# Performance work log

Hardware: AMD Instinct MI355X
Metric: run time of the kernel (lower is better)

Reference implementation:

```python
import jax, jax.numpy as jnp
import numpy as np

# ---- constants derived from init_kwargs ----
DETECT_THRESHOLD = 3.0
DETECT_SIGN = -1          # negative spikes
MARGIN_LEFT = 20          # snippet_T1
MARGIN_RIGHT = 20         # snippet_T2
CHANNEL_RADIUS = 100.0
SAMPLING_FREQUENCY = 30000.0
TIME_RADIUS = int(np.ceil(0.5 / 1000.0 * SAMPLING_FREQUENCY))  # = 15
MAX_DETECTIONS = 100000   # static cap for jit-compatible compaction


def setup_inputs() -> dict:
    key = jax.random.key(0)
    k1, k2 = jax.random.split(key)
    traces = jax.random.normal(k1, (150000, 384), dtype=jnp.float32)
    # spread channels over a 2000x2000 um area so radius=100 gives sparse adjacency
    channel_locations = jax.random.uniform(k2, (384, 2), dtype=jnp.float32) * 2000.0
    return {"traces": traces, "channel_locations": channel_locations}


def _detect_mask(traces, channel_locations):
    N, M = traces.shape
    # orientation (detect_sign < 0 -> traces_inv = -traces)
    if DETECT_SIGN > 0:
        traces_inv = traces
    elif DETECT_SIGN == 0:
        traces_inv = jnp.abs(traces)
    else:
        traces_inv = -traces

    # temporal max-pool, kernel 2*TR+1, stride 1, same padding (pads with -inf)
    pool = 2 * TIME_RADIUS + 1
    neg_inf = jnp.float32(-jnp.inf)
    temporal_max = jax.lax.reduce_window(
        traces_inv, neg_inf, jax.lax.max,
        window_dimensions=(pool, 1), window_strides=(1, 1),
        padding=((TIME_RADIUS, TIME_RADIUS), (0, 0)))  # [N, M]

    # channel adjacency from pairwise distances
    diff = channel_locations[:, None, :] - channel_locations[None, :, :]
    dists = jnp.sqrt(jnp.sum(diff * diff, axis=-1))  # [M, M]
    adj = dists <= CHANNEL_RADIUS

    # per-channel masked neighbor max over temporal_max columns -> [N, M]
    # sequential lax.map over channels avoids an N x M x M intermediate
    spatial_max = jax.lax.map(
        lambda row: jnp.max(jnp.where(row[None, :], temporal_max, neg_inf), axis=1),
        adj).T  # [N, M]

    t = jnp.arange(N)
    margin_ok = (t >= MARGIN_LEFT) & (t < N - MARGIN_RIGHT)  # [N]

    valid = ((traces_inv == temporal_max)
             & (traces_inv >= DETECT_THRESHOLD)
             & margin_ok[:, None]
             & (traces_inv >= spatial_max))
    return valid, traces_inv


def reference(traces, channel_locations):
    valid, _ = _detect_mask(traces, channel_locations)
    # row-major nonzero order == stable sort by time (row index)
    times, chans = jnp.nonzero(valid, size=MAX_DETECTIONS, fill_value=-1)
    return times.astype(jnp.int64), chans.astype(jnp.int32)
```

## Files before the change

### kernel.cpp

```cpp
#include <hip/hip_runtime.h>
#include <stdint.h>

#define M_CH       384
#define TR         15
#define MARGIN     20
#define CHUNK_ROWS 16
#define BM_WORDS   192
#define WPR        12

__device__ __forceinline__ uint32_t spread4(uint32_t x) {
    x = (x | (x << 12)) & 0x000F000Fu;
    x = (x | (x << 6))  & 0x03030303u;
    x = (x | (x << 3))  & 0x11111111u;
    return x;
}

__global__ void nbr_kernel(const float* __restrict__ locs,
                           uint32_t* __restrict__ nEntries,
                           uint8_t* __restrict__ entryWord,
                           uint32_t* __restrict__ entryMask) {
    __shared__ float lx[M_CH], ly[M_CH];
    int t = threadIdx.x;
    lx[t] = locs[2 * t];
    ly[t] = locs[2 * t + 1];
    __syncthreads();
    float x = lx[t], y = ly[t];
    uint32_t m[WPR];
    #pragma unroll
    for (int k = 0; k < WPR; ++k) m[k] = 0;
    for (int c = 0; c < M_CH; ++c) {
        float dx = x - lx[c], dy = y - ly[c];
        if (sqrtf(dx * dx + dy * dy) <= 100.0f) m[c >> 5] |= 1u << (c & 31);
    }
    int ne = 0;
    #pragma unroll
    for (int k = 0; k < WPR; ++k) {
        if (m[k]) {
            entryWord[t * WPR + ne] = (uint8_t)k;
            entryMask[t * WPR + ne] = m[k];
            ne++;
        }
    }
    nEntries[t] = (uint32_t)ne;
}

__global__ __launch_bounds__(256)
void cand_kernel(const float* __restrict__ traces, long n4, long nwords,
                 uint32_t* __restrict__ candWords) {
    const int lane = threadIdx.x & 63;
    const long wv = (((long)blockIdx.x * 256) + threadIdx.x) >> 6;
    const long fb = wv * 256;
    uint64_t B00,B01,B02,B03, B10,B11,B12,B13,
             B20,B21,B22,B23, B30,B31,B32,B33;
    {
        float4 v0 = make_float4(0,0,0,0), v1 = v0, v2 = v0, v3 = v0;
        long i0 = fb + 0 * 64 + lane;
        long i1 = fb + 1 * 64 + lane;
        long i2 = fb + 2 * 64 + lane;
        long i3 = fb + 3 * 64 + lane;
        if (i0 < n4) v0 = ((const float4*)traces)[i0];
        if (i1 < n4) v1 = ((const float4*)traces)[i1];
        if (i2 < n4) v2 = ((const float4*)traces)[i2];
        if (i3 < n4) v3 = ((const float4*)traces)[i3];
        B00 = __ballot(v0.x <= -3.0f); B01 = __ballot(v0.y <= -3.0f);
        B02 = __ballot(v0.z <= -3.0f); B03 = __ballot(v0.w <= -3.0f);
        B10 = __ballot(v1.x <= -3.0f); B11 = __ballot(v1.y <= -3.0f);
        B12 = __ballot(v1.z <= -3.0f); B13 = __ballot(v1.w <= -3.0f);
        B20 = __ballot(v2.x <= -3.0f); B21 = __ballot(v2.y <= -3.0f);
        B22 = __ballot(v2.z <= -3.0f); B23 = __ballot(v2.w <= -3.0f);
        B30 = __ballot(v3.x <= -3.0f); B31 = __ballot(v3.y <= -3.0f);
        B32 = __ballot(v3.z <= -3.0f); B33 = __ballot(v3.w <= -3.0f);
    }
    if (lane < 32) {
        int k  = lane >> 3;
        int sh = (lane & 7) * 8;
        uint64_t b0 = (k & 2) ? ((k & 1) ? B30 : B20) : ((k & 1) ? B10 : B00);
        uint64_t b1 = (k & 2) ? ((k & 1) ? B31 : B21) : ((k & 1) ? B11 : B01);
        uint64_t b2 = (k & 2) ? ((k & 1) ? B32 : B22) : ((k & 1) ? B12 : B02);
        uint64_t b3 = (k & 2) ? ((k & 1) ? B33 : B23) : ((k & 1) ? B13 : B03);
        uint32_t w = spread4((uint32_t)(b0 >> sh) & 0xFFu)
                   | (spread4((uint32_t)(b1 >> sh) & 0xFFu) << 1)
                   | (spread4((uint32_t)(b2 >> sh) & 0xFFu) << 2)
                   | (spread4((uint32_t)(b3 >> sh) & 0xFFu) << 3);
        long wIdx = wv * 32 + lane;
        if (wIdx < nwords) candWords[wIdx] = w;
    }
}

__global__ __launch_bounds__(192)
void validate_count_kernel(const float* __restrict__ traces, int N, long nwords,
                           const uint32_t* __restrict__ nEntries,
                           const uint8_t* __restrict__ entryWord,
                           const uint32_t* __restrict__ entryMask,
                           const uint32_t* __restrict__ candWords,
                           uint32_t* __restrict__ validOut,
                           uint32_t* __restrict__ chunkCounts) {
    __shared__ uint32_t red[3];
    const int t = threadIdx.x;
    const long w = (long)blockIdx.x * BM_WORDS + t;
    uint32_t out = 0;
    if (w < nwords) {
        uint32_t word = candWords[w];
        if (word) {
            int r  = (int)(w / WPR);
            int cw = (int)(w - (long)r * WPR);
            if (r >= MARGIN && r < N - MARGIN) {
                out = word;
                uint32_t tmp = word;
                while (tmp) {
                    int bit = __ffs(tmp) - 1;
                    tmp &= tmp - 1;
                    int c = cw * 32 + bit;
                    float raw = traces[(long)r * M_CH + c];
                    int ne = (int)nEntries[c];
                    bool bad = false;
                    for (int k = 0; k < ne; ++k) {
                        int wi = (int)entryWord[c * WPR + k];
                        uint32_t em = entryMask[c * WPR + k];
                        const uint32_t* colp = candWords + (long)(r - TR) * WPR + wi;
                        uint32_t hitRows = 0;
                        #pragma unroll
                        for (int dt = 0; dt < 31; ++dt) {
                            uint32_t h = colp[(long)dt * WPR] & em;
                            hitRows |= (h ? 1u : 0u) << dt;
                        }
                        if (hitRows) {
                            while (hitRows) {
                                int dt = __ffs(hitRows) - 1;
                                hitRows &= hitRows - 1;
                                uint32_t h = colp[(long)dt * WPR] & em;
                                while (h) {
                                    int b2 = __ffs(h) - 1;
                                    h &= h - 1;
                                    float v = traces[(long)(r - TR + dt) * M_CH + wi * 32 + b2];
                                    if (v < raw) bad = true;
                                }
                            }
                            if (bad) break;
                        }
                    }
                    if (bad) out &= ~(1u << bit);
                }
            }
        }
        validOut[w] = out;
    }
    int pc = __popc(out);
    #pragma unroll
    for (int off = 32; off; off >>= 1) pc += __shfl_xor(pc, off, 64);
    if ((t & 63) == 0) red[t >> 6] = (uint32_t)pc;
    __syncthreads();
    if (t == 0) chunkCounts[blockIdx.x] = red[0] + red[1] + red[2];
}

__global__ void scan_kernel(const uint32_t* __restrict__ counts, int n,
                            uint32_t* __restrict__ prefix) {
    __shared__ uint32_t s[256];
    int t = threadIdx.x;
    int per = (n + 255) / 256;
    int lo = t * per, hi = min(lo + per, n);
    uint32_t sum = 0;
    for (int i = lo; i < hi; ++i) sum += counts[i];
    s[t] = sum;
    __syncthreads();
    for (int off = 1; off < 256; off <<= 1) {
        uint32_t v = (t >= off) ? s[t - off] : 0;
        __syncthreads();
        s[t] += v;
        __syncthreads();
    }
    uint32_t run = s[t] - sum;
    for (int i = lo; i < hi; ++i) { prefix[i] = run; run += counts[i]; }
    if (t == 255) prefix[n] = run;
}

__global__ void emit_fill_kernel(const uint32_t* __restrict__ validOut,
                                 const uint32_t* __restrict__ chunkPrefix,
                                 int nchunk, int emitBlocks, int maxdet,
                                 int* __restrict__ times, int* __restrict__ chans) {
    if ((int)blockIdx.x >= emitBlocks) {
        int i = ((int)blockIdx.x - emitBlocks) * 256 + threadIdx.x;
        int total = (int)chunkPrefix[nchunk];
        if (i < maxdet && i >= total) { times[i] = -1; chans[i] = -1; }
        return;
    }
    int wv = threadIdx.x >> 6;
    int lane = threadIdx.x & 63;
    int chunkId = blockIdx.x * 4 + wv;
    if (chunkId >= nchunk) return;

    const uint32_t* wp = validOut + (long)chunkId * BM_WORDS + lane * 3;
    uint32_t b0 = wp[0], b1 = wp[1], b2 = wp[2];
    int local = __popc(b0) + __popc(b1) + __popc(b2);

    int s = local;
    #pragma unroll
    for (int off = 1; off < 64; off <<= 1) {
        int v = __shfl_up(s, off, 64);
        if (lane >= off) s += v;
    }
    int base = (int)chunkPrefix[chunkId] + (s - local);
    int r0 = chunkId * CHUNK_ROWS;

    uint32_t words[3] = { b0, b1, b2 };
    #pragma unroll
    for (int q = 0; q < 3; ++q) {
        uint32_t x = words[q];
        int fbase = (lane * 3 + q) * 32;
        while (x) {
            int b = __ffs(x) - 1;
            x &= x - 1;
            int f = fbase + b;
            int n = f / M_CH;
            int ch = f - n * M_CH;
            if (base < maxdet) {
                times[base] = r0 + n;
                chans[base] = ch;
            }
            base++;
        }
    }
}

extern "C" void kernel_launch(void* const* d_in, const int* in_sizes, int n_in,
                              void* d_out, int out_size, void* d_ws, size_t ws_size,
                              hipStream_t stream) {
    const float* traces = (const float*)d_in[0];
    const float* locs   = (const float*)d_in[1];
    const int M = M_CH;
    const int N = in_sizes[0] / M;
    const long nsamp = (long)N * M;
    const int maxdet = out_size / 2;
    int* times = (int*)d_out;
    int* chans = times + maxdet;

    const long n4     = nsamp / 4;
    const long nwords = nsamp / 32;
    const int  nchunk = (N + CHUNK_ROWS - 1) / CHUNK_ROWS;

    char* ws = (char*)d_ws;
    uint32_t* nEntries    = (uint32_t*)(ws + 0);
    uint8_t*  entryWord   = (uint8_t*)(ws + 1536);
    uint32_t* entryMask   = (uint32_t*)(ws + 6144);
    uint32_t* chunkCounts = (uint32_t*)(ws + 24576);
    uint32_t* chunkPrefix = (uint32_t*)(ws + 62080);
    uint32_t* candWords   = (uint32_t*)(ws + 99584);
    uint32_t* validOut    = (uint32_t*)(ws + 7299584);

    nbr_kernel<<<1, M_CH, 0, stream>>>(locs, nEntries, entryWord, entryMask);

    const long nwaves = (nwords + 31) / 32;
    const int  cblocks = (int)((nwaves + 3) / 4);
    cand_kernel<<<cblocks, 256, 0, stream>>>(traces, n4, nwords, candWords);

    validate_count_kernel<<<nchunk, BM_WORDS, 0, stream>>>(
        traces, N, nwords, nEntries, entryWord, entryMask, candWords,
        validOut, chunkCounts);

    scan_kernel<<<1, 256, 0, stream>>>(chunkCounts, nchunk, chunkPrefix);

    const int emitBlocks = (nchunk + 3) / 4;
    const int fillBlocks = (maxdet + 255) / 256;
    emit_fill_kernel<<<emitBlocks + fillBlocks, 256, 0, stream>>>(
        validOut, chunkPrefix, nchunk, emitBlocks, maxdet, times, chans);
}
```

Baseline: 425.7 us.

## Stage candidate window in LDS, skip self-only checks, fuse neighbor build into cand kernel

The neighbor-mask computation is folded into an extra block of the candidate kernel, which removes one kernel launch. The validate kernel now stages a 46-row window of candidate bitmap words in shared memory and reads neighbourhood bits from there instead of from global memory. It also first ORs all neighbor bits, excluding the sample itself, so that it loads trace values only when a competing candidate exists. This saves launch overhead and global bitmap traffic, at the cost of slightly more shared memory per block and a two-pass loop over neighbor entries.

```diff
diff --git a/kernel.cpp b/kernel.cpp
--- a/kernel.cpp
+++ b/kernel.cpp
@@ -7,6 +7,7 @@
 #define CHUNK_ROWS 16
 #define BM_WORDS   192
 #define WPR        12
+#define WIN_ROWS   46
 
 __device__ __forceinline__ uint32_t spread4(uint32_t x) {
     x = (x | (x << 12)) & 0x000F000Fu;
@@ -15,38 +16,44 @@
     return x;
 }
 
-__global__ void nbr_kernel(const float* __restrict__ locs,
-                           uint32_t* __restrict__ nEntries,
-                           uint8_t* __restrict__ entryWord,
-                           uint32_t* __restrict__ entryMask) {
-    __shared__ float lx[M_CH], ly[M_CH];
-    int t = threadIdx.x;
-    lx[t] = locs[2 * t];
-    ly[t] = locs[2 * t + 1];
-    __syncthreads();
-    float x = lx[t], y = ly[t];
-    uint32_t m[WPR];
-    #pragma unroll
-    for (int k = 0; k < WPR; ++k) m[k] = 0;
-    for (int c = 0; c < M_CH; ++c) {
-        float dx = x - lx[c], dy = y - ly[c];
-        if (sqrtf(dx * dx + dy * dy) <= 100.0f) m[c >> 5] |= 1u << (c & 31);
-    }
-    int ne = 0;
-    #pragma unroll
-    for (int k = 0; k < WPR; ++k) {
-        if (m[k]) {
-            entryWord[t * WPR + ne] = (uint8_t)k;
-            entryMask[t * WPR + ne] = m[k];
-            ne++;
-        }
-    }
-    nEntries[t] = (uint32_t)ne;
-}
-
 __global__ __launch_bounds__(256)
-void cand_kernel(const float* __restrict__ traces, long n4, long nwords,
-                 uint32_t* __restrict__ candWords) {
+void cand_kernel(const float* __restrict__ traces,
+                 const float* __restrict__ locs,
+                 long n4, long nwords, int nbrBlock,
+                 uint32_t* __restrict__ candWords,
+                 uint32_t* __restrict__ nEntries,
+                 uint8_t* __restrict__ entryWord,
+                 uint32_t* __restrict__ entryMask) {
+    if ((int)blockIdx.x >= nbrBlock) {
+        __shared__ float lx[M_CH], ly[M_CH];
+        const int t = threadIdx.x;
+        for (int c = t; c < M_CH; c += 256) {
+            lx[c] = locs[2 * c];
+            ly[c] = locs[2 * c + 1];
+        }
+        __syncthreads();
+        for (int c0 = t; c0 < M_CH; c0 += 256) {
+            float x = lx[c0], y = ly[c0];
+            int ne = 0;
+            for (int k = 0; k < WPR; ++k) {
+                uint32_t mk = 0;
+                #pragma unroll
+                for (int b = 0; b < 32; ++b) {
+                    int c = k * 32 + b;
+                    float dx = x - lx[c], dy = y - ly[c];
+                    if (sqrtf(dx * dx + dy * dy) <= 100.0f) mk |= 1u << b;
+                }
+                if (mk) {
+                    entryWord[c0 * WPR + ne] = (uint8_t)k;
+                    entryMask[c0 * WPR + ne] = mk;
+                    ne++;
+                }
+            }
+            nEntries[c0] = (uint32_t)ne;
+        }
+        return;
+    }
+
     const int lane = threadIdx.x & 63;
     const long wv = (((long)blockIdx.x * 256) + threadIdx.x) >> 6;
     const long fb = wv * 256;
@@ -95,51 +102,77 @@
                            const uint32_t* __restrict__ candWords,
                            uint32_t* __restrict__ validOut,
                            uint32_t* __restrict__ chunkCounts) {
+    __shared__ uint32_t win[WIN_ROWS * WPR];
     __shared__ uint32_t red[3];
     const int t = threadIdx.x;
+    const int r0 = (int)blockIdx.x * CHUNK_ROWS;
+
+    {
+        const long base = (long)(r0 - TR) * WPR;
+        #pragma unroll
+        for (int i0 = 0; i0 < WIN_ROWS * WPR; i0 += 192) {
+            int i = i0 + t;
+            if (i < WIN_ROWS * WPR) {
+                long g = base + i;
+                win[i] = (g >= 0 && g < nwords) ? candWords[g] : 0u;
+            }
+        }
+    }
+    __syncthreads();
+
+    const int lr = t / WPR;
+    const int wi = t - lr * WPR;
+    const int r  = r0 + lr;
     const long w = (long)blockIdx.x * BM_WORDS + t;
+
     uint32_t out = 0;
     if (w < nwords) {
-        uint32_t word = candWords[w];
-        if (word) {
-            int r  = (int)(w / WPR);
-            int cw = (int)(w - (long)r * WPR);
-            if (r >= MARGIN && r < N - MARGIN) {
-                out = word;
-                uint32_t tmp = word;
-                while (tmp) {
-                    int bit = __ffs(tmp) - 1;
-                    tmp &= tmp - 1;
-                    int c = cw * 32 + bit;
+        uint32_t word = win[(lr + TR) * WPR + wi];
+        if (word && r >= MARGIN && r < N - MARGIN) {
+            out = word;
+            uint32_t tmp = word;
+            while (tmp) {
+                int bit = __ffs(tmp) - 1;
+                tmp &= tmp - 1;
+                const int c = wi * 32 + bit;
+                const uint32_t selfbit = 1u << bit;
+                const int ne = (int)nEntries[c];
+
+                uint32_t anyComp = 0;
+                for (int k = 0; k < ne; ++k) {
+                    int wiE = (int)entryWord[c * WPR + k];
+                    uint32_t em = entryMask[c * WPR + k];
+                    const uint32_t* colp = &win[lr * WPR + wiE];
+                    uint32_t orw = 0;
+                    #pragma unroll
+                    for (int dt = 0; dt < 31; ++dt) {
+                        uint32_t h = colp[dt * WPR];
+                        if (dt == TR) h &= (wiE == wi) ? ~selfbit : 0xFFFFFFFFu;
+                        orw |= h & em;
+                    }
+                    anyComp |= orw;
+                }
+
+                if (anyComp) {
                     float raw = traces[(long)r * M_CH + c];
-                    int ne = (int)nEntries[c];
                     bool bad = false;
-                    for (int k = 0; k < ne; ++k) {
-                        int wi = (int)entryWord[c * WPR + k];
+                    for (int k = 0; k < ne && !bad; ++k) {
+                        int wiE = (int)entryWord[c * WPR + k];
                         uint32_t em = entryMask[c * WPR + k];
-                        const uint32_t* colp = candWords + (long)(r - TR) * WPR + wi;
-                        uint32_t hitRows = 0;
+                        const uint32_t* colp = &win[lr * WPR + wiE];
                         #pragma unroll
                         for (int dt = 0; dt < 31; ++dt) {
-                            uint32_t h = colp[(long)dt * WPR] & em;
-                            hitRows |= (h ? 1u : 0u) << dt;
-                        }
-                        if (hitRows) {
-                            while (hitRows) {
-                                int dt = __ffs(hitRows) - 1;
-                                hitRows &= hitRows - 1;
-                                uint32_t h = colp[(long)dt * WPR] & em;
-                                while (h) {
-                                    int b2 = __ffs(h) - 1;
-                                    h &= h - 1;
-                                    float v = traces[(long)(r - TR + dt) * M_CH + wi * 32 + b2];
-                                    if (v < raw) bad = true;
-                                }
+                            uint32_t h = colp[dt * WPR] & em;
+                            if (dt == TR && wiE == wi) h &= ~selfbit;
+                            while (h) {
+                                int b2 = __ffs(h) - 1;
+                                h &= h - 1;
+                                float v = traces[(long)(r - TR + dt) * M_CH + wiE * 32 + b2];
+                                if (v < raw) bad = true;
                             }
-                            if (bad) break;
                         }
                     }
-                    if (bad) out &= ~(1u << bit);
+                    if (bad) out &= ~selfbit;
                 }
             }
         }
@@ -247,11 +280,11 @@
     uint32_t* candWords   = (uint32_t*)(ws + 99584);
     uint32_t* validOut    = (uint32_t*)(ws + 7299584);
 
-    nbr_kernel<<<1, M_CH, 0, stream>>>(locs, nEntries, entryWord, entryMask);
-
     const long nwaves = (nwords + 31) / 32;
     const int  cblocks = (int)((nwaves + 3) / 4);
-    cand_kernel<<<cblocks, 256, 0, stream>>>(traces, n4, nwords, candWords);
+    cand_kernel<<<cblocks + 1, 256, 0, stream>>>(
+        traces, locs, n4, nwords, cblocks,
+        candWords, nEntries, entryWord, entryMask);
 
     validate_count_kernel<<<nchunk, BM_WORDS, 0, stream>>>(
         traces, N, nwords, nEntries, entryWord, entryMask, candWords,
```

Result: slower. 449.3 us (+5.5%).
